# Kernel optimization log

Measured on AMD Instinct MI355X. Metric: run time of the kernel, lower is better.

Reference implementation:

```python
import jax, jax.numpy as jnp
import numpy as np


def setup_inputs() -> dict:
    key = jax.random.key(0)
    k1, k2 = jax.random.split(key)
    # x: (b, t, C, H, W) feature maps
    x = jax.random.normal(k1, (2, 32, 128, 64, 64), dtype=jnp.float32)
    # attn_mask: (n_heads, b, t, t, h, w) attention weights at coarse resolution
    attn_mask = jax.random.uniform(k2, (4, 2, 32, 32, 16, 16), dtype=jnp.float32)
    return {"x": x, "attn_mask": attn_mask}


def reference(x, attn_mask):
    # TemporalAggregationMode.ATT_GROUP, pad_mask=None branch.
    g, b, t, _, h, w = attn_mask.shape
    B, T, C, H, W = x.shape
    c = C // g  # channels per head-group

    attn = attn_mask.reshape(g * b * t, t, h, w)
    if H > w:
        # bilinear upsample, half-pixel centers == torch align_corners=False
        attn = jax.image.resize(attn, (g * b * t, t, H, W), method='bilinear')
    else:
        k = w // H  # AvgPool2d(kernel_size=k), stride=k
        attn = attn.reshape(g * b * t, t, H, k, W, k).mean(axis=(3, 5))
    attn = attn.reshape(g, b, t, t, H, W)

    # x.chunk(n_heads, dim=2): contiguous channel groups -> (b, t, g, c, H, W)
    xg = x.reshape(b, t, g, c, H, W)

    # out[g,b,q,c,h,w] = sum_k attn[g,b,q,k,h,w] * xg[b,k,g,c,h,w]
    # fused per-pixel temporal contraction (no (g,b,t,t,c,H,W) blowup)
    out = jnp.einsum('gbqkhw,bkgchw->bqgchw', attn, xg)

    # torch.cat over groups along channel dim == reshape groups back into C
    return out.reshape(b, t, C, H, W)
```

## Files before the change

### kernel.cpp

```cpp
#include <hip/hip_runtime.h>

typedef float f4 __attribute__((ext_vector_type(4)));

#define Gn 4
#define Bn 2
#define Tn 32
#define Cn 128
#define CG 32
#define Hn 64
#define Wn 64
#define HC 16
#define WC 16

#define QT 16
#define APAD 20

__global__ __launch_bounds__(256, 4)
void temporal_agg_kernel(const float* __restrict__ x,
                         const float* __restrict__ attn,
                         float* __restrict__ out) {
    const int bid   = blockIdx.x;
    const int qt    = (bid >> 3) & 1;
    const int pair  = ((bid >> 4) << 3) | (bid & 7);
    const int whalf = pair & 1;
    const int h     = (pair >> 1) & 63;
    const int b     = (pair >> 7) & 1;
    const int g     = pair >> 8;

    const int tid = threadIdx.x;

    const float chf = 0.25f * (float)h - 0.375f;
    const float h0f = floorf(chf);
    const float fh  = chf - h0f;
    int h0 = (int)h0f;
    int h1 = h0 + 1;
    h0 = min(max(h0, 0), HC - 1);
    h1 = min(max(h1, 0), HC - 1);

    __shared__ float Ah[Tn][10][APAD];

    const int wcb = whalf * 8 - 1;
    const float* abase = attn + (size_t)(g * Bn + b) * (Tn * Tn * HC * WC)
                              + (size_t)(qt * QT) * (Tn * HC * WC);
    #pragma unroll 8
    for (int i = 0; i < 32; ++i) {
        int idx = tid + 256 * i;
        int wc = idx & 15;
        int k  = (idx >> 4) & 31;
        int q  = idx >> 9;
        const float* p = abase + (size_t)(q * Tn + k) * (HC * WC);
        float v0 = p[h0 * WC + wc];
        float v1 = p[h1 * WC + wc];
        float ah = v0 + fh * (v1 - v0);
        int j = wc - wcb;
        if (j >= 0 && j < 10) Ah[k][j][q] = ah;
        if (whalf == 0 && wc == 0)  Ah[k][0][q] = ah;
        if (whalf == 1 && wc == 15) Ah[k][9][q] = ah;
    }
    __syncthreads();

    const int qslot = tid & 3;
    const int wl    = (tid >> 2) & 7;
    const int cslot = tid >> 5;
    const int q0    = qslot * 4;
    const int wfine = whalf * 32 + wl * 4;
    const int off_hw = h * Wn + wfine;

    f4 acc[4][4];
    #pragma unroll
    for (int qq = 0; qq < 4; ++qq)
        #pragma unroll
        for (int cc = 0; cc < 4; ++cc)
            acc[qq][cc] = (f4)0.0f;

    const int cbase = g * CG + cslot * 4;
    const float* xb = x + (size_t)b * (Tn * Cn * Hn * Wn)
                        + (size_t)cbase * (Hn * Wn) + off_hw;

    #pragma unroll 2
    for (int k = 0; k < Tn; ++k) {
        f4 t0 = *(const f4*)&Ah[k][wl    ][q0];
        f4 t1 = *(const f4*)&Ah[k][wl + 1][q0];
        f4 t2 = *(const f4*)&Ah[k][wl + 2][q0];

        f4 xv[4];
        const float* xk = xb + (size_t)k * (Cn * Hn * Wn);
        #pragma unroll
        for (int cc = 0; cc < 4; ++cc)
            xv[cc] = *(const f4*)(xk + cc * (Hn * Wn));

        #pragma unroll
        for (int qq = 0; qq < 4; ++qq) {
            f4 a;
            a.x = 0.375f * t0[qq] + 0.625f * t1[qq];
            a.y = 0.125f * t0[qq] + 0.875f * t1[qq];
            a.z = 0.875f * t1[qq] + 0.125f * t2[qq];
            a.w = 0.625f * t1[qq] + 0.375f * t2[qq];
            #pragma unroll
            for (int cc = 0; cc < 4; ++cc)
                acc[qq][cc] += a * xv[cc];
        }
    }

    #pragma unroll
    for (int qq = 0; qq < 4; ++qq) {
        const int q = qt * QT + q0 + qq;
        float* ob = out + ((size_t)(b * Tn + q) * Cn + cbase) * (Hn * Wn) + off_hw;
        #pragma unroll
        for (int cc = 0; cc < 4; ++cc)
            *(f4*)(ob + cc * (Hn * Wn)) = acc[qq][cc];
    }
}

extern "C" void kernel_launch(void* const* d_in, const int* in_sizes, int n_in,
                              void* d_out, int out_size, void* d_ws, size_t ws_size,
                              hipStream_t stream) {
    const float* x    = (const float*)d_in[0];
    const float* attn = (const float*)d_in[1];
    float* out        = (float*)d_out;
    temporal_agg_kernel<<<dim3(Gn * Bn * Hn * 2 * 2), dim3(256), 0, stream>>>(x, attn, out);
}
```

Baseline: 322.4 us.

## Prefetch x tiles into LDS with an async multi-slot global_load_lds pipeline

Replaces the direct per-thread global loads of x inside the temporal loop with asynchronous global_load_lds staging into a 5-slot LDS ring buffer, issued 4 timesteps ahead. Each wave stages only the channels it consumes, and hand-placed s_waitcnt instructions order the async copies against the LDS reads, so no block-wide barrier is needed. The query mapping is changed to a strided layout (qsl + 4*i), which changes the LDS access pattern into the attention table. The goal is to hide global memory latency. In exchange it uses more LDS, lowers the occupancy hint from 4 to 3 blocks, and relies on fragile manual wait counts.

```diff
diff --git a/kernel.cpp b/kernel.cpp
--- a/kernel.cpp
+++ b/kernel.cpp
@@ -1,6 +1,8 @@
 #include <hip/hip_runtime.h>
 
 typedef float f4 __attribute__((ext_vector_type(4)));
+typedef const __attribute__((address_space(1))) void gas_t;
+typedef __attribute__((address_space(3))) void las_t;
 
 #define Gn 4
 #define Bn 2
@@ -14,8 +16,10 @@
 
 #define QT 16
 #define APAD 20
+#define NSLOT 5
+#define DEPTH 4
 
-__global__ __launch_bounds__(256, 4)
+__global__ __launch_bounds__(256, 3)
 void temporal_agg_kernel(const float* __restrict__ x,
                          const float* __restrict__ attn,
                          float* __restrict__ out) {
@@ -27,7 +31,22 @@
     const int b     = (pair >> 7) & 1;
     const int g     = pair >> 8;
 
-    const int tid = threadIdx.x;
+    const int tid  = threadIdx.x;
+    const int lane = tid & 63;
+    const int wid  = tid >> 6;
+
+    __shared__ float Ah[Tn][10][APAD];
+    __shared__ float Xs[NSLOT][CG][32];
+
+    const int c_ld = 8 * wid + (lane >> 3);
+    const float* xsrc = x + ((size_t)(b * Tn) * Cn + (g * CG + c_ld)) * (Hn * Wn)
+                          + h * Wn + whalf * 32 + (lane & 7) * 4;
+
+#define STAGE(k_, slot_) \
+    __builtin_amdgcn_global_load_lds((gas_t*)(xsrc + (size_t)(k_) * (Cn * Hn * Wn)), \
+                                     (las_t*)&Xs[slot_][8 * wid][0], 16, 0, 0)
+
+    STAGE(0, 0); STAGE(1, 1); STAGE(2, 2); STAGE(3, 3);
 
     const float chf = 0.25f * (float)h - 0.375f;
     const float h0f = floorf(chf);
@@ -36,8 +55,6 @@
     int h1 = h0 + 1;
     h0 = min(max(h0, 0), HC - 1);
     h1 = min(max(h1, 0), HC - 1);
-
-    __shared__ float Ah[Tn][10][APAD];
 
     const int wcb = whalf * 8 - 1;
     const float* abase = attn + (size_t)(g * Bn + b) * (Tn * Tn * HC * WC)
@@ -59,10 +76,9 @@
     }
     __syncthreads();
 
-    const int qslot = tid & 3;
+    const int qsl   = tid & 3;
     const int wl    = (tid >> 2) & 7;
     const int cslot = tid >> 5;
-    const int q0    = qslot * 4;
     const int wfine = whalf * 32 + wl * 4;
     const int off_hw = h * Wn + wfine;
 
@@ -73,21 +89,18 @@
         for (int cc = 0; cc < 4; ++cc)
             acc[qq][cc] = (f4)0.0f;
 
-    const int cbase = g * CG + cslot * 4;
-    const float* xb = x + (size_t)b * (Tn * Cn * Hn * Wn)
-                        + (size_t)cbase * (Hn * Wn) + off_hw;
-
-    #pragma unroll 2
-    for (int k = 0; k < Tn; ++k) {
-        f4 t0 = *(const f4*)&Ah[k][wl    ][q0];
-        f4 t1 = *(const f4*)&Ah[k][wl + 1][q0];
-        f4 t2 = *(const f4*)&Ah[k][wl + 2][q0];
-
+    auto body = [&](int k, int cur) {
+        float t0[4], t1[4], t2[4];
+        #pragma unroll
+        for (int i = 0; i < 4; ++i) {
+            t0[i] = Ah[k][wl    ][qsl + 4 * i];
+            t1[i] = Ah[k][wl + 1][qsl + 4 * i];
+            t2[i] = Ah[k][wl + 2][qsl + 4 * i];
+        }
         f4 xv[4];
-        const float* xk = xb + (size_t)k * (Cn * Hn * Wn);
         #pragma unroll
         for (int cc = 0; cc < 4; ++cc)
-            xv[cc] = *(const f4*)(xk + cc * (Hn * Wn));
+            xv[cc] = *(const f4*)&Xs[cur][cslot * 4 + cc][wl * 4];
 
         #pragma unroll
         for (int qq = 0; qq < 4; ++qq) {
@@ -100,16 +113,33 @@
             for (int cc = 0; cc < 4; ++cc)
                 acc[qq][cc] += a * xv[cc];
         }
+    };
+
+    int cur = 0;
+    for (int k = 0; k < Tn - DEPTH; ++k) {
+        asm volatile("s_waitcnt vmcnt(3)" ::: "memory");
+        body(k, cur);
+        asm volatile("s_waitcnt lgkmcnt(0)" ::: "memory");
+        const int ws = (cur == 0) ? (NSLOT - 1) : (cur - 1);
+        STAGE(k + DEPTH, ws);
+        cur = (cur == NSLOT - 1) ? 0 : cur + 1;
+    }
+    asm volatile("s_waitcnt vmcnt(0)" ::: "memory");
+    for (int k = Tn - DEPTH; k < Tn; ++k) {
+        body(k, cur);
+        cur = (cur == NSLOT - 1) ? 0 : cur + 1;
     }
 
+    const int cbase = g * CG + cslot * 4;
     #pragma unroll
     for (int qq = 0; qq < 4; ++qq) {
-        const int q = qt * QT + q0 + qq;
+        const int q = qt * QT + qsl + 4 * qq;
         float* ob = out + ((size_t)(b * Tn + q) * Cn + cbase) * (Hn * Wn) + off_hw;
         #pragma unroll
         for (int cc = 0; cc < 4; ++cc)
             *(f4*)(ob + cc * (Hn * Wn)) = acc[qq][cc];
     }
+#undef STAGE
 }
 
 extern "C" void kernel_launch(void* const* d_in, const int* in_sizes, int n_in,
```

Result: faster. 296.7 us (-8.0%).

## Prefetch next-timestep x in registers and interleave query mapping across threads

Applied to the files above, without the earlier changes.

Issues the first x loads before the attention staging phase, so global latency overlaps the shared-memory fill. Inside the temporal loop, it double-buffers the x vectors by loading step k+1 while computing step k. It also changes each thread's query assignment from a contiguous block of 4 to a stride-4 pattern, which replaces vector LDS reads with scalar ones, possibly to reduce bank conflicts. The extra buffers add register pressure, which may hurt occupancy under the launch bounds.

```diff
diff --git a/kernel.cpp b/kernel.cpp
--- a/kernel.cpp
+++ b/kernel.cpp
@@ -29,6 +29,22 @@
 
     const int tid = threadIdx.x;
 
+    __shared__ float Ah[Tn][10][APAD];
+
+    const int qsl   = tid & 3;
+    const int wl    = (tid >> 2) & 7;
+    const int cslot = tid >> 5;
+    const int wfine = whalf * 32 + wl * 4;
+    const int off_hw = h * Wn + wfine;
+    const int cbase = g * CG + cslot * 4;
+    const float* xb = x + (size_t)b * (Tn * Cn * Hn * Wn)
+                        + (size_t)cbase * (Hn * Wn) + off_hw;
+
+    f4 xcur[4], xnxt[4];
+    #pragma unroll
+    for (int cc = 0; cc < 4; ++cc)
+        xcur[cc] = *(const f4*)(xb + cc * (Hn * Wn));
+
     const float chf = 0.25f * (float)h - 0.375f;
     const float h0f = floorf(chf);
     const float fh  = chf - h0f;
@@ -36,8 +52,6 @@
     int h1 = h0 + 1;
     h0 = min(max(h0, 0), HC - 1);
     h1 = min(max(h1, 0), HC - 1);
-
-    __shared__ float Ah[Tn][10][APAD];
 
     const int wcb = whalf * 8 - 1;
     const float* abase = attn + (size_t)(g * Bn + b) * (Tn * Tn * HC * WC)
@@ -59,13 +73,6 @@
     }
     __syncthreads();
 
-    const int qslot = tid & 3;
-    const int wl    = (tid >> 2) & 7;
-    const int cslot = tid >> 5;
-    const int q0    = qslot * 4;
-    const int wfine = whalf * 32 + wl * 4;
-    const int off_hw = h * Wn + wfine;
-
     f4 acc[4][4];
     #pragma unroll
     for (int qq = 0; qq < 4; ++qq)
@@ -73,21 +80,22 @@
         for (int cc = 0; cc < 4; ++cc)
             acc[qq][cc] = (f4)0.0f;
 
-    const int cbase = g * CG + cslot * 4;
-    const float* xb = x + (size_t)b * (Tn * Cn * Hn * Wn)
-                        + (size_t)cbase * (Hn * Wn) + off_hw;
-
     #pragma unroll 2
     for (int k = 0; k < Tn; ++k) {
-        f4 t0 = *(const f4*)&Ah[k][wl    ][q0];
-        f4 t1 = *(const f4*)&Ah[k][wl + 1][q0];
-        f4 t2 = *(const f4*)&Ah[k][wl + 2][q0];
+        if (k + 1 < Tn) {
+            const float* xn = xb + (size_t)(k + 1) * (Cn * Hn * Wn);
+            #pragma unroll
+            for (int cc = 0; cc < 4; ++cc)
+                xnxt[cc] = *(const f4*)(xn + cc * (Hn * Wn));
+        }
 
-        f4 xv[4];
-        const float* xk = xb + (size_t)k * (Cn * Hn * Wn);
+        float t0[4], t1[4], t2[4];
         #pragma unroll
-        for (int cc = 0; cc < 4; ++cc)
-            xv[cc] = *(const f4*)(xk + cc * (Hn * Wn));
+        for (int i = 0; i < 4; ++i) {
+            t0[i] = Ah[k][wl    ][qsl + 4 * i];
+            t1[i] = Ah[k][wl + 1][qsl + 4 * i];
+            t2[i] = Ah[k][wl + 2][qsl + 4 * i];
+        }
 
         #pragma unroll
         for (int qq = 0; qq < 4; ++qq) {
@@ -98,13 +106,19 @@
             a.w = 0.625f * t1[qq] + 0.375f * t2[qq];
             #pragma unroll
             for (int cc = 0; cc < 4; ++cc)
-                acc[qq][cc] += a * xv[cc];
+                acc[qq][cc] += a * xcur[cc];
+        }
+
+        if (k + 1 < Tn) {
+            #pragma unroll
+            for (int cc = 0; cc < 4; ++cc)
+                xcur[cc] = xnxt[cc];
         }
     }
 
     #pragma unroll
     for (int qq = 0; qq < 4; ++qq) {
-        const int q = qt * QT + q0 + qq;
+        const int q = qt * QT + qsl + 4 * qq;
         float* ob = out + ((size_t)(b * Tn + q) * Cn + cbase) * (Hn * Wn) + off_hw;
         #pragma unroll
         for (int cc = 0; cc < 4; ++cc)
```

Result: slower. 609.4 us (+89.0%).
